# Kernel optimization log

Hardware: AMD Instinct MI355X
Metric: run time of the kernel (lower is better)

Reference implementation:

```python
import jax, jax.numpy as jnp
import numpy as np

D = 1024       # d_model
H = 16         # total heads
HD = 64        # k_dim per head
HL = 8         # local heads (block-local attention)
STRIDE = 128   # block size
C = 32         # summary columns per block for global heads
DFF = 4096
EPS = 1e-6
NEG = -1e9


def layernorm(x, g, b):
    mu = jnp.mean(x, axis=-1, keepdims=True)
    var = jnp.mean(jnp.square(x - mu), axis=-1, keepdims=True)
    return g * (x - mu) / jnp.sqrt(var + EPS) + b


def setup_inputs() -> dict:
    key = jax.random.key(0)
    ks = jax.random.split(key, 16)
    B, S = 4, 4096
    s = 0.02
    inp = {
        "src": jax.random.normal(ks[0], (B, S, D), jnp.float32),
        "input_mask": jnp.ones((B, S), dtype=bool),
        "Wq": jax.random.normal(ks[1], (D, H * HD), jnp.float32) * s,
        "bq": jnp.zeros((H * HD,), jnp.float32),
        "Wk": jax.random.normal(ks[2], (D, H * HD), jnp.float32) * s,
        "bk": jnp.zeros((H * HD,), jnp.float32),
        "Wv": jax.random.normal(ks[3], (D, H * HD), jnp.float32) * s,
        "bv": jnp.zeros((H * HD,), jnp.float32),
        "Wo": jax.random.normal(ks[4], (H * HD, D), jnp.float32) * s,
        "bo": jnp.zeros((D,), jnp.float32),
        "ln1_g": jnp.ones((D,), jnp.float32),
        "ln1_b": jnp.zeros((D,), jnp.float32),
        "W1": jax.random.normal(ks[5], (D, DFF), jnp.float32) * s,
        "b1": jnp.zeros((DFF,), jnp.float32),
        "W2": jax.random.normal(ks[6], (DFF, D), jnp.float32) * s,
        "b2": jnp.zeros((D,), jnp.float32),
        "ln2_g": jnp.ones((D,), jnp.float32),
        "ln2_b": jnp.zeros((D,), jnp.float32),
    }
    return inp


def sparse_attention(src, input_mask, Wq, bq, Wk, bk, Wv, bv, Wo, bo):
    B, S, _ = src.shape
    nb = S // STRIDE
    scale = HD ** -0.5
    q = (src @ Wq + bq).reshape(B, S, H, HD)
    k = (src @ Wk + bk).reshape(B, S, H, HD)
    v = (src @ Wv + bv).reshape(B, S, H, HD)

    # ---- local heads: attend within their own block of length STRIDE ----
    ql = q[:, :, :HL].reshape(B, nb, STRIDE, HL, HD)
    kl = k[:, :, :HL].reshape(B, nb, STRIDE, HL, HD)
    vl = v[:, :, :HL].reshape(B, nb, STRIDE, HL, HD)
    sl = jnp.einsum('bnqhd,bnkhd->bnhqk', ql, kl) * scale
    mloc = input_mask.reshape(B, nb, 1, 1, STRIDE)
    sl = jnp.where(mloc, sl, NEG)
    al = jax.nn.softmax(sl, axis=-1)
    ol = jnp.einsum('bnhqk,bnkhd->bnqhd', al, vl).reshape(B, S, HL, HD)

    # ---- global heads: attend to last C positions of every block (fixed pattern) ----
    idx = np.nonzero(np.arange(S) % STRIDE >= STRIDE - C)[0]  # static, nb*C keys
    kg = k[:, idx, HL:]                        # [B, nb*C, HG, HD]
    vg = v[:, idx, HL:]
    sg = jnp.einsum('bqhd,bkhd->bhqk', q[:, :, HL:], kg) * scale
    mg = input_mask[:, idx][:, None, None, :]
    sg = jnp.where(mg, sg, NEG)
    ag = jax.nn.softmax(sg, axis=-1)
    og = jnp.einsum('bhqk,bkhd->bqhd', ag, vg)  # [B, S, HG, HD]

    out = jnp.concatenate([ol, og], axis=2).reshape(B, S, H * HD)
    return out @ Wo + bo


def reference(src, input_mask, Wq, bq, Wk, bk, Wv, bv, Wo, bo,
              ln1_g, ln1_b, W1, b1, W2, b2, ln2_g, ln2_b):
    temp = sparse_attention(src, input_mask, Wq, bq, Wk, bk, Wv, bv, Wo, bo)
    attn = layernorm(src + temp, ln1_g, ln1_b)
    ffn = jax.nn.relu(attn @ W1 + b1) @ W2 + b2
    state = layernorm(attn + ffn, ln2_g, ln2_b)
    return state
```

## Files before the change

kernel.cpp:

```cpp
#include <hip/hip_runtime.h>
#include <hip/hip_bf16.h>
#include <stdint.h>


typedef unsigned short bf16_t;
typedef __attribute__((ext_vector_type(8))) short short8;
typedef __attribute__((ext_vector_type(4))) float v4f;

static __device__ __forceinline__ unsigned short f2b(float f) {
    unsigned int x = __float_as_uint(f);
    x += 0x7fffu + ((x >> 16) & 1u);
    return (unsigned short)(x >> 16);
}
static __device__ __forceinline__ float b2f(unsigned short u) {
    return __uint_as_float(((unsigned int)u) << 16);
}

static __device__ __forceinline__ void gload16(const void* g, void* l) {
    __builtin_amdgcn_global_load_lds(
        (const __attribute__((address_space(1))) uint32_t*)g,
        (__attribute__((address_space(3))) uint32_t*)l, 16, 0, 0);
}

template<int N>
static __device__ __forceinline__ void vmwait() {
    asm volatile("s_waitcnt vmcnt(%0)" :: "n"(N) : "memory");
}


__global__ __launch_bounds__(256) void transpose_convert(
    const float* __restrict__ W, bf16_t* __restrict__ Wt, int K, int N) {
    __shared__ float tile[32][33];
    int n0 = blockIdx.x * 32, k0 = blockIdx.y * 32;
    int tx = threadIdx.x, ty = threadIdx.y;
    for (int i = ty; i < 32; i += 8)
        tile[i][tx] = W[(size_t)(k0 + i) * N + n0 + tx];
    __syncthreads();
    for (int i = ty; i < 32; i += 8)
        Wt[(size_t)(n0 + i) * K + k0 + tx] = f2b(tile[tx][i]);
}

__global__ __launch_bounds__(256) void f32_to_bf16_vec(
    const float* __restrict__ in, bf16_t* __restrict__ out, int n4) {
    int i = blockIdx.x * blockDim.x + threadIdx.x;
    if (i >= n4) return;
    float4 v = ((const float4*)in)[i];
    uint2 p;
    p.x = (unsigned)f2b(v.x) | ((unsigned)f2b(v.y) << 16);
    p.y = (unsigned)f2b(v.z) | ((unsigned)f2b(v.w) << 16);
    ((uint2*)out)[i] = p;
}

template<int BN>
__global__ __launch_bounds__(512, 2) void gemm_bt(
    const bf16_t* __restrict__ A, const bf16_t* __restrict__ Bt,
    const float* __restrict__ bias, const float* __restrict__ bias2,
    const float* __restrict__ bias3, const float* __restrict__ resf,
    const bf16_t* __restrict__ resb, float* __restrict__ Cf,
    bf16_t* __restrict__ Cb, int N, int K, int relu) {
    constexpr int N_REP = BN / 64;
    constexpr int BLD = BN / 128;
    constexpr int LPT = 2 + BLD;
    constexpr int ASH = 8192;
    constexpr int TSH = ASH + BN * 32;
    __shared__ bf16_t lds[4][TSH];

    int t = threadIdx.x;
    int lane = t & 63;
    int wave = t >> 6;
    int wm = (wave >> 2) * 128;
    int wn = (wave & 3) * (BN / 4);
    int m0 = blockIdx.x * 256, n0 = blockIdx.y * BN;

    size_t aoff[2]; int adst[2];
#pragma unroll
    for (int p = 0; p < 2; ++p) {
        int u = p * 512 + t;
        int row = ((u >> 6) << 4) + (lane & 15);
        int kk = ((u >> 4) & 3) * 8;
        aoff[p] = (size_t)(m0 + row) * K + kk;
        adst[p] = (u & ~63) * 8;
    }
    size_t boff[BLD]; int bdst[BLD];
#pragma unroll
    for (int p = 0; p < BLD; ++p) {
        int u = p * 512 + t;
        int row = ((u >> 6) << 4) + (lane & 15);
        int kk = ((u >> 4) & 3) * 8;
        boff[p] = (size_t)(n0 + row) * K + kk;
        bdst[p] = (u & ~63) * 8;
    }

    auto stage = [&](int buf, int kt) {
        int k0 = kt * 32;
#pragma unroll
        for (int p = 0; p < 2; ++p)
            gload16(A + aoff[p] + k0, &lds[buf][adst[p]]);
#pragma unroll
        for (int p = 0; p < BLD; ++p)
            gload16(Bt + boff[p] + k0, &lds[buf][ASH + bdst[p]]);
    };

    v4f acc[8][N_REP];
#pragma unroll
    for (int i = 0; i < 8; ++i)
#pragma unroll
        for (int j = 0; j < N_REP; ++j) acc[i][j] = {0.f, 0.f, 0.f, 0.f};

    int NT = K >> 5;
    stage(0, 0); stage(1, 1); stage(2, 2);

    int aro = (wm >> 4) * 512 + lane * 8;
    int bro = ASH + (wn >> 4) * 512 + lane * 8;

    for (int it = 0; it < NT; ++it) {
        int ahead = NT - 1 - it;
        if (ahead >= 2) vmwait<2 * LPT>();
        else if (ahead == 1) vmwait<LPT>();
        else vmwait<0>();
        __builtin_amdgcn_s_barrier();
        __builtin_amdgcn_sched_barrier(0);

        int cb = it & 3;
        short8 fA[8], fB[N_REP];
#pragma unroll
        for (int i = 0; i < 8; ++i)
            fA[i] = *(const short8*)&lds[cb][aro + i * 512];
#pragma unroll
        for (int j = 0; j < N_REP; ++j)
            fB[j] = *(const short8*)&lds[cb][bro + j * 512];

        if (it + 3 < NT) stage((it + 3) & 3, it + 3);

        __builtin_amdgcn_s_setprio(1);
#pragma unroll
        for (int i = 0; i < 8; ++i)
#pragma unroll
            for (int j = 0; j < N_REP; ++j)
                acc[i][j] = __builtin_amdgcn_mfma_f32_16x16x32_bf16(fA[i], fB[j], acc[i][j], 0, 0, 0);
        __builtin_amdgcn_s_setprio(0);
    }

    int qrow = (lane >> 4) * 4;
    int c15 = lane & 15;
#pragma unroll
    for (int i = 0; i < 8; ++i) {
#pragma unroll
        for (int j = 0; j < N_REP; ++j) {
            int col = n0 + wn + j * 16 + c15;
            float bval;
            if (bias2) {
                int seg = col >> 10;
                const float* bp = seg == 0 ? bias : (seg == 1 ? bias2 : bias3);
                bval = bp[col & 1023];
            } else {
                bval = bias[col];
            }
#pragma unroll
            for (int r = 0; r < 4; ++r) {
                int row = m0 + wm + i * 16 + qrow + r;
                size_t idx = (size_t)row * N + col;
                float val = acc[i][j][r] + bval;
                if (resf) val += resf[idx];
                if (resb) val += b2f(resb[idx]);
                if (relu) val = fmaxf(val, 0.f);
                if (Cf) Cf[idx] = val;
                if (Cb) Cb[idx] = f2b(val);
            }
        }
    }
}

template<int NCHUNK, bool GLOBAL>
__global__ __launch_bounds__(256) void mfma_attn(
    const bf16_t* __restrict__ qkv, bf16_t* __restrict__ o, int head_base) {
    __shared__ bf16_t buf[32768];
    bf16_t* ldsQ  = buf;
    bf16_t* ldsP  = buf;
    bf16_t* ldsK  = buf + 16384;
    bf16_t* ldsVt = buf + 24576;

    int qc = blockIdx.x, hh = blockIdx.y, b = blockIdx.z;
    int h = head_base + hh;
    int t = threadIdx.x, lane = t & 63, w = t >> 6;
    int quad = lane >> 4, c15 = lane & 15;
    size_t base = (size_t)b * 4096 * 3072 + (size_t)h * 64;

#pragma unroll
    for (int u = t; u < 1024; u += 256) {
        int s = u >> 9, mt = (u >> 6) & 7, qq = (u >> 4) & 3, l = u & 15;
        int tok = qc * 128 + mt * 16 + l;
        gload16(qkv + base + (size_t)tok * 3072 + s * 32 + qq * 8, ldsQ + (u & ~63) * 8);
    }
    __syncthreads();

    short8 fQ[2][2];
#pragma unroll
    for (int i = 0; i < 2; ++i)
#pragma unroll
        for (int s = 0; s < 2; ++s)
            fQ[i][s] = *(const short8*)(ldsQ + (s * 512 + (w * 2 + i) * 64 + lane) * 8);

    v4f oacc[2][4];
    float lacc[2][4];
#pragma unroll
    for (int i = 0; i < 2; ++i)
#pragma unroll
        for (int n = 0; n < 4; ++n) oacc[i][n] = {0.f, 0.f, 0.f, 0.f};
#pragma unroll
    for (int i = 0; i < 2; ++i)
#pragma unroll
        for (int r = 0; r < 4; ++r) lacc[i][r] = 0.f;

    for (int c = 0; c < NCHUNK; ++c) {
        __syncthreads();
#pragma unroll
        for (int u = t; u < 1024; u += 256) {
            int s = u >> 9, nt = (u >> 6) & 7, qq = (u >> 4) & 3, l = u & 15;
            int key = c * 128 + nt * 16 + l;
            int tok = GLOBAL ? ((key >> 5) * 128 + 96 + (key & 31)) : (qc * 128 + key);
            gload16(qkv + base + 1024 + (size_t)tok * 3072 + s * 32 + qq * 8, ldsK + (u & ~63) * 8);
        }
#pragma unroll
        for (int u = t; u < 1024; u += 256) {
            int tt = u >> 8, nt = (u >> 6) & 3, qq = (u >> 4) & 3, l = u & 15;
            int d = nt * 16 + l;
            int key0 = c * 128 + tt * 32 + qq * 8;
            int tok0 = GLOBAL ? ((key0 >> 5) * 128 + 96 + (key0 & 31)) : (qc * 128 + key0);
            const bf16_t* vp = qkv + base + 2048 + (size_t)tok0 * 3072 + d;
            short8 tmp;
#pragma unroll
            for (int jj = 0; jj < 8; ++jj) tmp[jj] = (short)vp[(size_t)jj * 3072];
            *(short8*)(ldsVt + u * 8) = tmp;
        }
        __syncthreads();

        v4f sacc[2][8];
#pragma unroll
        for (int i = 0; i < 2; ++i)
#pragma unroll
            for (int j = 0; j < 8; ++j) sacc[i][j] = {0.f, 0.f, 0.f, 0.f};
#pragma unroll
        for (int s = 0; s < 2; ++s)
#pragma unroll
            for (int j = 0; j < 8; ++j) {
                short8 fK = *(const short8*)(ldsK + (s * 512 + j * 64 + lane) * 8);
#pragma unroll
                for (int i = 0; i < 2; ++i)
                    sacc[i][j] = __builtin_amdgcn_mfma_f32_16x16x32_bf16(fQ[i][s], fK, sacc[i][j], 0, 0, 0);
            }

#pragma unroll
        for (int i = 0; i < 2; ++i) {
            float rs[4] = {0.f, 0.f, 0.f, 0.f};
#pragma unroll
            for (int j = 0; j < 8; ++j)
#pragma unroll
                for (int r = 0; r < 4; ++r) {
                    float p = __expf(sacc[i][j][r] * 0.125f);
                    sacc[i][j][r] = p;
                    rs[r] += p;
                }
#pragma unroll
            for (int m = 1; m < 16; m <<= 1)
#pragma unroll
                for (int r = 0; r < 4; ++r) rs[r] += __shfl_xor(rs[r], m);
#pragma unroll
            for (int r = 0; r < 4; ++r) lacc[i][r] += rs[r];
#pragma unroll
            for (int j = 0; j < 8; ++j) {
                int tt = j >> 1;
                int qq = (2 * j + (c15 >> 3)) & 3;
#pragma unroll
                for (int r = 0; r < 4; ++r) {
                    int slot = (quad * 4 + r) ^ qq;
                    int unit = (w * 4 + tt) * 128 + i * 64 + qq * 16 + slot;
                    ldsP[unit * 8 + (c15 & 7)] = f2b(sacc[i][j][r]);
                }
            }
        }

#pragma unroll
        for (int tt = 0; tt < 4; ++tt) {
            short8 fP[2];
#pragma unroll
            for (int i = 0; i < 2; ++i)
                fP[i] = *(const short8*)(ldsP + (((w * 4 + tt) * 128 + i * 64
                              + quad * 16 + (c15 ^ quad))) * 8);
#pragma unroll
            for (int n = 0; n < 4; ++n) {
                short8 fV = *(const short8*)(ldsVt + (tt * 256 + n * 64 + lane) * 8);
#pragma unroll
                for (int i = 0; i < 2; ++i)
                    oacc[i][n] = __builtin_amdgcn_mfma_f32_16x16x32_bf16(fP[i], fV, oacc[i][n], 0, 0, 0);
            }
        }
    }

#pragma unroll
    for (int i = 0; i < 2; ++i)
#pragma unroll
        for (int r = 0; r < 4; ++r) {
            int row = qc * 128 + (w * 2 + i) * 16 + quad * 4 + r;
            float inv = 1.f / lacc[i][r];
            bf16_t* orow = o + ((size_t)b * 4096 + row) * 1024 + h * 64;
#pragma unroll
            for (int n = 0; n < 4; ++n)
                orow[n * 16 + c15] = f2b(oacc[i][n][r] * inv);
        }
}

__global__ __launch_bounds__(256) void ln_kernel(
    const float* x, const float* g, const float* bta,
    float* outf, bf16_t* outb) {
    int row = blockIdx.x, t = threadIdx.x;
    const float4 vv = ((const float4*)(x + (size_t)row * 1024))[t];
    float s = vv.x + vv.y + vv.z + vv.w;
    float ss = vv.x * vv.x + vv.y * vv.y + vv.z * vv.z + vv.w * vv.w;
    for (int off = 32; off > 0; off >>= 1) {
        s += __shfl_down(s, off);
        ss += __shfl_down(ss, off);
    }
    __shared__ float red[8];
    int wave = t >> 6;
    if ((t & 63) == 0) { red[wave] = s; red[wave + 4] = ss; }
    __syncthreads();
    float ts = red[0] + red[1] + red[2] + red[3];
    float tss = red[4] + red[5] + red[6] + red[7];
    float mu = ts * (1.f / 1024.f);
    float var = tss * (1.f / 1024.f) - mu * mu;
    float rstd = rsqrtf(var + 1e-6f);
    float4 gv = ((const float4*)g)[t];
    float4 bv = ((const float4*)bta)[t];
    float4 ov;
    ov.x = (vv.x - mu) * rstd * gv.x + bv.x;
    ov.y = (vv.y - mu) * rstd * gv.y + bv.y;
    ov.z = (vv.z - mu) * rstd * gv.z + bv.z;
    ov.w = (vv.w - mu) * rstd * gv.w + bv.w;
    if (outf) ((float4*)(outf + (size_t)row * 1024))[t] = ov;
    if (outb) {
        uint2 pk;
        pk.x = (unsigned)f2b(ov.x) | ((unsigned)f2b(ov.y) << 16);
        pk.y = (unsigned)f2b(ov.z) | ((unsigned)f2b(ov.w) << 16);
        ((uint2*)(outb + (size_t)row * 1024))[t] = pk;
    }
}

extern "C" void kernel_launch(void* const* d_in, const int* in_sizes, int n_in,
                              void* d_out, int out_size, void* d_ws, size_t ws_size,
                              hipStream_t stream) {
    const float* src = (const float*)d_in[0];
    const float* Wq = (const float*)d_in[2];  const float* bq = (const float*)d_in[3];
    const float* Wk = (const float*)d_in[4];  const float* bk = (const float*)d_in[5];
    const float* Wv = (const float*)d_in[6];  const float* bv = (const float*)d_in[7];
    const float* Wo = (const float*)d_in[8];  const float* bo = (const float*)d_in[9];
    const float* g1 = (const float*)d_in[10]; const float* be1 = (const float*)d_in[11];
    const float* W1 = (const float*)d_in[12]; const float* b1 = (const float*)d_in[13];
    const float* W2 = (const float*)d_in[14]; const float* b2 = (const float*)d_in[15];
    const float* g2 = (const float*)d_in[16]; const float* be2 = (const float*)d_in[17];
    float* out = (float*)d_out;
    char* ws = (char*)d_ws;
    const size_t MB = 1ull << 20;

    bf16_t* xb    = (bf16_t*)(ws + 0 * MB);
    bf16_t* ob    = (bf16_t*)(ws + 0 * MB);
    bf16_t* alnb  = (bf16_t*)(ws + 0 * MB);
    bf16_t* qkv   = (bf16_t*)(ws + 32 * MB);
    bf16_t* hb    = (bf16_t*)(ws + 32 * MB);
    bf16_t* wqkvt = (bf16_t*)(ws + 128 * MB);
    bf16_t* wot   = (bf16_t*)(ws + 134 * MB);
    bf16_t* w1t   = (bf16_t*)(ws + 136 * MB);
    bf16_t* w2t   = (bf16_t*)(ws + 144 * MB);

    dim3 tb(32, 8);
    transpose_convert<<<dim3(32, 32), tb, 0, stream>>>(Wq, wqkvt, 1024, 1024);
    transpose_convert<<<dim3(32, 32), tb, 0, stream>>>(Wk, wqkvt + 1024 * 1024, 1024, 1024);
    transpose_convert<<<dim3(32, 32), tb, 0, stream>>>(Wv, wqkvt + 2 * 1024 * 1024, 1024, 1024);
    transpose_convert<<<dim3(32, 32), tb, 0, stream>>>(Wo, wot, 1024, 1024);
    transpose_convert<<<dim3(128, 32), tb, 0, stream>>>(W1, w1t, 1024, 4096);
    transpose_convert<<<dim3(32, 128), tb, 0, stream>>>(W2, w2t, 4096, 1024);
    f32_to_bf16_vec<<<16384, 256, 0, stream>>>(src, xb, 4194304);

    gemm_bt<256><<<dim3(64, 12), 512, 0, stream>>>(xb, wqkvt, bq, bk, bv,
        nullptr, nullptr, nullptr, qkv, 3072, 1024, 0);

    mfma_attn<1, false><<<dim3(32, 8, 4), 256, 0, stream>>>(qkv, ob, 0);
    mfma_attn<8, true ><<<dim3(32, 8, 4), 256, 0, stream>>>(qkv, ob, 8);

    gemm_bt<256><<<dim3(64, 4), 512, 0, stream>>>(ob, wot, bo, nullptr, nullptr,
        src, nullptr, out, nullptr, 1024, 1024, 0);
    ln_kernel<<<16384, 256, 0, stream>>>(out, g1, be1, nullptr, alnb);

    for (int mc = 0; mc < 2; ++mc) {
        const bf16_t* arows = alnb + (size_t)mc * 8192 * 1024;
        float* yrows = out + (size_t)mc * 8192 * 1024;
        gemm_bt<256><<<dim3(32, 16), 512, 0, stream>>>(arows, w1t, b1, nullptr, nullptr,
            nullptr, nullptr, nullptr, hb, 4096, 1024, 1);
        gemm_bt<128><<<dim3(32, 8), 512, 0, stream>>>(hb, w2t, b2, nullptr, nullptr,
            nullptr, arows, yrows, nullptr, 1024, 4096, 0);
    }
    ln_kernel<<<16384, 256, 0, stream>>>(out, g2, be2, out, nullptr);

    (void)in_sizes; (void)n_in; (void)out_size; (void)ws_size;
}
```

Baseline: 1.033 ms.

## Pre-transpose V and pipeline attention K/V loads with triple-buffered LDS

Adds a separate kernel that transposes V into a contiguous per-head layout, so attention can load V tiles with direct global-to-LDS 16-byte loads instead of strided scalar gathers. Attention now processes 64-key chunks with a three-stage LDS ring, prefetching two chunks ahead using vmcnt waits and bare barriers, and raises wave priority around MFMA sections. This aims to hide load latency and remove the uncoalesced V gather, at the cost of an extra transpose pass, more workspace traffic, and twice as many loop iterations.

```diff
diff --git a/kernel.cpp b/kernel.cpp
--- a/kernel.cpp
+++ b/kernel.cpp
@@ -25,6 +25,9 @@
 template<int N>
 static __device__ __forceinline__ void vmwait() {
     asm volatile("s_waitcnt vmcnt(%0)" :: "n"(N) : "memory");
+}
+static __device__ __forceinline__ void lgkmwait0() {
+    asm volatile("s_waitcnt lgkmcnt(0)" ::: "memory");
 }
 
 
@@ -49,6 +52,33 @@
     p.x = (unsigned)f2b(v.x) | ((unsigned)f2b(v.y) << 16);
     p.y = (unsigned)f2b(v.z) | ((unsigned)f2b(v.w) << 16);
     ((uint2*)out)[i] = p;
+}
+
+template<bool GLOBAL>
+__global__ __launch_bounds__(256) void v_transpose(
+    const bf16_t* __restrict__ qkv, bf16_t* __restrict__ vt, int ntok) {
+    __shared__ bf16_t tile[4096];
+    int tb = blockIdx.x, h = blockIdx.y, b = blockIdx.z;
+    int t = threadIdx.x;
+    size_t src = (size_t)b * 4096 * 3072 + (size_t)(GLOBAL ? h + 8 : h) * 64 + 2048;
+    for (int u = t; u < 512; u += 256) {
+        int row = u >> 3, g = u & 7;
+        int lt = tb * 64 + row;
+        int tok = GLOBAL ? ((lt >> 5) * 128 + 96 + (lt & 31)) : lt;
+        short8 vrow = *(const short8*)(qkv + src + (size_t)tok * 3072 + g * 8);
+        *(short8*)&tile[(row * 8 + (g ^ (row >> 3))) * 8] = vrow;
+    }
+    __syncthreads();
+    for (int u = t; u < 512; u += 256) {
+        int d = u >> 3, t8g = u & 7;
+        short8 vcol;
+#pragma unroll
+        for (int j = 0; j < 8; ++j) {
+            int row = t8g * 8 + j;
+            vcol[j] = tile[(row * 8 + ((d >> 3) ^ (row >> 3))) * 8 + (d & 7)];
+        }
+        *(short8*)(vt + ((size_t)(b * 8 + h) * 64 + d) * ntok + (size_t)tb * 64 + t8g * 8) = vcol;
+    }
 }
 
 template<int BN>
@@ -173,26 +203,65 @@
 
 template<int NCHUNK, bool GLOBAL>
 __global__ __launch_bounds__(256) void mfma_attn(
-    const bf16_t* __restrict__ qkv, bf16_t* __restrict__ o, int head_base) {
+    const bf16_t* __restrict__ qkv, const bf16_t* __restrict__ vt,
+    bf16_t* __restrict__ o, int head_base) {
     __shared__ bf16_t buf[32768];
-    bf16_t* ldsQ  = buf;
-    bf16_t* ldsP  = buf;
-    bf16_t* ldsK  = buf + 16384;
-    bf16_t* ldsVt = buf + 24576;
+    bf16_t* ldsQ = buf;
+    bf16_t* ldsP = buf;
+    constexpr int KB = 8192, VB = 20480;
 
     int qc = blockIdx.x, hh = blockIdx.y, b = blockIdx.z;
     int h = head_base + hh;
     int t = threadIdx.x, lane = t & 63, w = t >> 6;
     int quad = lane >> 4, c15 = lane & 15;
     size_t base = (size_t)b * 4096 * 3072 + (size_t)h * 64;
+    const int NTOK = GLOBAL ? 1024 : 4096;
+    size_t vtbase = (size_t)(b * 8 + hh) * 64 * NTOK + (GLOBAL ? 0 : (size_t)qc * 128);
+    const int CADV = (GLOBAL ? 256 : 64) * 3072;
+
+    size_t koff[2]; int kdst[2];
+#pragma unroll
+    for (int p = 0; p < 2; ++p) {
+        int u = p * 256 + t;
+        int s = u >> 8;
+        int kl = ((u >> 6) & 3) * 16 + (lane & 15);
+        int dk = s * 32 + ((lane >> 4) & 3) * 8;
+        int tok0 = GLOBAL ? ((kl >> 5) * 128 + 96 + (kl & 31)) : (qc * 128 + kl);
+        koff[p] = base + 1024 + (size_t)tok0 * 3072 + dk;
+        kdst[p] = KB + (u & ~63) * 8;
+    }
+    size_t voff[2]; int vdst[2];
+#pragma unroll
+    for (int p = 0; p < 2; ++p) {
+        int u = p * 256 + t;
+        int dd = ((u >> 6) & 3) * 16 + (lane & 15);
+        int kl = (u >> 8) * 32 + ((lane >> 4) & 3) * 8;
+        voff[p] = vtbase + (size_t)dd * NTOK + kl;
+        vdst[p] = VB + (u & ~63) * 8;
+    }
+
+    auto stage = [&](int c) {
+        int q = c % 3;
+        size_t ka = (size_t)c * CADV;
+        size_t va = (size_t)c * 64;
+#pragma unroll
+        for (int p = 0; p < 2; ++p)
+            gload16(qkv + koff[p] + ka, buf + kdst[p] + q * 4096);
+#pragma unroll
+        for (int p = 0; p < 2; ++p)
+            gload16(vt + voff[p] + va, buf + vdst[p] + q * 4096);
+    };
 
 #pragma unroll
     for (int u = t; u < 1024; u += 256) {
-        int s = u >> 9, mt = (u >> 6) & 7, qq = (u >> 4) & 3, l = u & 15;
-        int tok = qc * 128 + mt * 16 + l;
+        int s = u >> 9, mt = (u >> 6) & 7, qq = (u >> 4) & 3, ll = u & 15;
+        int tok = qc * 128 + mt * 16 + ll;
         gload16(qkv + base + (size_t)tok * 3072 + s * 32 + qq * 8, ldsQ + (u & ~63) * 8);
     }
-    __syncthreads();
+    stage(0);
+    stage(1);
+    vmwait<8>();
+    __builtin_amdgcn_s_barrier();
 
     short8 fQ[2][2];
 #pragma unroll
@@ -200,6 +269,8 @@
 #pragma unroll
         for (int s = 0; s < 2; ++s)
             fQ[i][s] = *(const short8*)(ldsQ + (s * 512 + (w * 2 + i) * 64 + lane) * 8);
+    lgkmwait0();
+    __builtin_amdgcn_sched_barrier(0);
 
     v4f oacc[2][4];
     float lacc[2][4];
@@ -213,48 +284,37 @@
         for (int r = 0; r < 4; ++r) lacc[i][r] = 0.f;
 
     for (int c = 0; c < NCHUNK; ++c) {
-        __syncthreads();
-#pragma unroll
-        for (int u = t; u < 1024; u += 256) {
-            int s = u >> 9, nt = (u >> 6) & 7, qq = (u >> 4) & 3, l = u & 15;
-            int key = c * 128 + nt * 16 + l;
-            int tok = GLOBAL ? ((key >> 5) * 128 + 96 + (key & 31)) : (qc * 128 + key);
-            gload16(qkv + base + 1024 + (size_t)tok * 3072 + s * 32 + qq * 8, ldsK + (u & ~63) * 8);
-        }
-#pragma unroll
-        for (int u = t; u < 1024; u += 256) {
-            int tt = u >> 8, nt = (u >> 6) & 3, qq = (u >> 4) & 3, l = u & 15;
-            int d = nt * 16 + l;
-            int key0 = c * 128 + tt * 32 + qq * 8;
-            int tok0 = GLOBAL ? ((key0 >> 5) * 128 + 96 + (key0 & 31)) : (qc * 128 + key0);
-            const bf16_t* vp = qkv + base + 2048 + (size_t)tok0 * 3072 + d;
-            short8 tmp;
-#pragma unroll
-            for (int jj = 0; jj < 8; ++jj) tmp[jj] = (short)vp[(size_t)jj * 3072];
-            *(short8*)(ldsVt + u * 8) = tmp;
-        }
-        __syncthreads();
-
-        v4f sacc[2][8];
+        if (c + 1 < NCHUNK) vmwait<4>();
+        else vmwait<0>();
+        __builtin_amdgcn_s_barrier();
+        __builtin_amdgcn_sched_barrier(0);
+        if (c + 2 < NCHUNK) stage(c + 2);
+
+        const bf16_t* Kq = buf + KB + (c % 3) * 4096;
+        const bf16_t* Vq = buf + VB + (c % 3) * 4096;
+
+        v4f sacc[2][4];
 #pragma unroll
         for (int i = 0; i < 2; ++i)
 #pragma unroll
-            for (int j = 0; j < 8; ++j) sacc[i][j] = {0.f, 0.f, 0.f, 0.f};
+            for (int j = 0; j < 4; ++j) sacc[i][j] = {0.f, 0.f, 0.f, 0.f};
+        __builtin_amdgcn_s_setprio(1);
 #pragma unroll
         for (int s = 0; s < 2; ++s)
 #pragma unroll
-            for (int j = 0; j < 8; ++j) {
-                short8 fK = *(const short8*)(ldsK + (s * 512 + j * 64 + lane) * 8);
+            for (int j = 0; j < 4; ++j) {
+                short8 fK = *(const short8*)(Kq + (s * 256 + j * 64 + lane) * 8);
 #pragma unroll
                 for (int i = 0; i < 2; ++i)
                     sacc[i][j] = __builtin_amdgcn_mfma_f32_16x16x32_bf16(fQ[i][s], fK, sacc[i][j], 0, 0, 0);
             }
+        __builtin_amdgcn_s_setprio(0);
 
 #pragma unroll
         for (int i = 0; i < 2; ++i) {
             float rs[4] = {0.f, 0.f, 0.f, 0.f};
 #pragma unroll
-            for (int j = 0; j < 8; ++j)
+            for (int j = 0; j < 4; ++j)
 #pragma unroll
                 for (int r = 0; r < 4; ++r) {
                     float p = __expf(sacc[i][j][r] * 0.125f);
@@ -268,33 +328,35 @@
 #pragma unroll
             for (int r = 0; r < 4; ++r) lacc[i][r] += rs[r];
 #pragma unroll
-            for (int j = 0; j < 8; ++j) {
+            for (int j = 0; j < 4; ++j) {
                 int tt = j >> 1;
                 int qq = (2 * j + (c15 >> 3)) & 3;
 #pragma unroll
                 for (int r = 0; r < 4; ++r) {
                     int slot = (quad * 4 + r) ^ qq;
-                    int unit = (w * 4 + tt) * 128 + i * 64 + qq * 16 + slot;
+                    int unit = (w * 2 + tt) * 128 + i * 64 + qq * 16 + slot;
                     ldsP[unit * 8 + (c15 & 7)] = f2b(sacc[i][j][r]);
                 }
             }
         }
 
-#pragma unroll
-        for (int tt = 0; tt < 4; ++tt) {
+        __builtin_amdgcn_s_setprio(1);
+#pragma unroll
+        for (int tt = 0; tt < 2; ++tt) {
             short8 fP[2];
 #pragma unroll
             for (int i = 0; i < 2; ++i)
-                fP[i] = *(const short8*)(ldsP + (((w * 4 + tt) * 128 + i * 64
-                              + quad * 16 + (c15 ^ quad))) * 8);
+                fP[i] = *(const short8*)(ldsP + ((w * 2 + tt) * 128 + i * 64
+                              + quad * 16 + (c15 ^ quad)) * 8);
 #pragma unroll
             for (int n = 0; n < 4; ++n) {
-                short8 fV = *(const short8*)(ldsVt + (tt * 256 + n * 64 + lane) * 8);
+                short8 fV = *(const short8*)(Vq + (tt * 256 + n * 64 + lane) * 8);
 #pragma unroll
                 for (int i = 0; i < 2; ++i)
                     oacc[i][n] = __builtin_amdgcn_mfma_f32_16x16x32_bf16(fP[i], fV, oacc[i][n], 0, 0, 0);
             }
         }
+        __builtin_amdgcn_s_setprio(0);
     }
 
 #pragma unroll
@@ -371,6 +433,8 @@
     bf16_t* wot   = (bf16_t*)(ws + 134 * MB);
     bf16_t* w1t   = (bf16_t*)(ws + 136 * MB);
     bf16_t* w2t   = (bf16_t*)(ws + 144 * MB);
+    bf16_t* vt_l  = (bf16_t*)(ws + 152 * MB);
+    bf16_t* vt_g  = (bf16_t*)(ws + 168 * MB);
 
     dim3 tb(32, 8);
     transpose_convert<<<dim3(32, 32), tb, 0, stream>>>(Wq, wqkvt, 1024, 1024);
@@ -384,8 +448,11 @@
     gemm_bt<256><<<dim3(64, 12), 512, 0, stream>>>(xb, wqkvt, bq, bk, bv,
         nullptr, nullptr, nullptr, qkv, 3072, 1024, 0);
 
-    mfma_attn<1, false><<<dim3(32, 8, 4), 256, 0, stream>>>(qkv, ob, 0);
-    mfma_attn<8, true ><<<dim3(32, 8, 4), 256, 0, stream>>>(qkv, ob, 8);
+    v_transpose<false><<<dim3(64, 8, 4), 256, 0, stream>>>(qkv, vt_l, 4096);
+    v_transpose<true ><<<dim3(16, 8, 4), 256, 0, stream>>>(qkv, vt_g, 1024);
+
+    mfma_attn<2,  false><<<dim3(32, 8, 4), 256, 0, stream>>>(qkv, vt_l, ob, 0);
+    mfma_attn<16, true ><<<dim3(32, 8, 4), 256, 0, stream>>>(qkv, vt_g, ob, 8);
 
     gemm_bt<256><<<dim3(64, 4), 512, 0, stream>>>(ob, wot, bo, nullptr, nullptr,
         src, nullptr, out, nullptr, 1024, 1024, 0);
```

After: 988.8 us. 4.3% less time.
